# Kernel optimization log

Measured on AMD Instinct MI355X. Metric: run time of the kernel, lower is better.

Reference implementation:

```python
import jax, jax.numpy as jnp
import numpy as np

N_NODES = 100000
N_EDGES = 3200000
D_FEAT = 256
UNITS = 256


def setup_inputs() -> dict:
    key = jax.random.key(0)
    k1, k2, k3, k4, k5 = jax.random.split(key, 5)
    edge_row = jax.random.randint(k1, (N_EDGES,), 0, N_NODES, dtype=jnp.int32)
    edge_col = jax.random.randint(k2, (N_EDGES,), 0, N_NODES, dtype=jnp.int32)
    edge_val = jax.random.uniform(k3, (N_EDGES,), dtype=jnp.float32)
    x = jax.random.normal(k4, (N_NODES, D_FEAT), dtype=jnp.float32)
    weight = jax.random.normal(k5, (D_FEAT, UNITS), dtype=jnp.float32) * (1.0 / np.sqrt(D_FEAT))
    bias = jnp.zeros((UNITS,), dtype=jnp.float32)
    return {"edge_row": edge_row, "edge_col": edge_col, "edge_val": edge_val,
            "x": x, "weight": weight, "bias": bias}


def reference(edge_row, edge_col, edge_val, x, weight, bias):
    # h = X @ W  -- dense feature transform (N, units)
    h = x @ weight
    # out = An @ h -- SpMM over COO adjacency: out[r] += val_e * h[c_e]
    msgs = edge_val[:, None] * h[edge_col]          # (E, units) gather + scale
    out = jax.ops.segment_sum(msgs, edge_row, num_segments=N_NODES)
    out = out + bias
    return jax.nn.relu(out)
```

## Files before the change

### kernel.cpp

```cpp
#include <hip/hip_runtime.h>
#include <hip/hip_bf16.h>

#define N_NODES 100000
#define N_EDGES 3200000
#define DFEAT 256
#define UNITS 256

#define CHUNK 512
#define CHUNK_SHIFT 9
#define NCHUNKS ((N_NODES + CHUNK - 1) / CHUNK)

#define BIN_TILE 2048
#define BIN_NWG ((N_EDGES + BIN_TILE - 1) / BIN_TILE)
#define PADC 208

typedef short bf16x8 __attribute__((ext_vector_type(8)));
typedef float f32x4 __attribute__((ext_vector_type(4)));

__device__ __forceinline__ unsigned short f2bf(float f) {
    union { float f; unsigned u; } v; v.f = f;
    unsigned u = v.u;
    u += 0x7FFFu + ((u >> 16) & 1u);
    return (unsigned short)(u >> 16);
}

__global__ __launch_bounds__(256) void convert_x(const float4* __restrict__ x4,
                                                 unsigned short* __restrict__ xh) {
    size_t i = (size_t)blockIdx.x * 256 + threadIdx.x;
    float4 v = x4[i];
    ushort4 o = make_ushort4(f2bf(v.x), f2bf(v.y), f2bf(v.z), f2bf(v.w));
    *(ushort4*)&xh[i * 4] = o;
}

__global__ void convert_w(const float* __restrict__ w, unsigned short* __restrict__ wt) {
    int n = blockIdx.x, k = threadIdx.x;
    wt[n * DFEAT + k] = f2bf(w[k * UNITS + n]);
}

__global__ __launch_bounds__(256) void chunk_hist(const int* __restrict__ erow,
                                                  int* __restrict__ hist_all) {
    __shared__ int h[256];
    const int tid = threadIdx.x;
    h[tid] = 0;
    __syncthreads();
    const int base = blockIdx.x * BIN_TILE;
#pragma unroll
    for (int j = 0; j < 8; ++j) {
        int e = base + j * 256 + tid;
        if (e < N_EDGES) atomicAdd(&h[erow[e] >> CHUNK_SHIFT], 1);
    }
    __syncthreads();
    if (tid < NCHUNKS) hist_all[blockIdx.x * PADC + tid] = h[tid];
}

__global__ __launch_bounds__(256) void col_scan(int* __restrict__ hist_all,
                                                int* __restrict__ chunk_cnt) {
    __shared__ int t[256];
    const int b = blockIdx.x;
    const int tid = threadIdx.x;
    int v[7]; int local = 0;
#pragma unroll
    for (int j = 0; j < 7; ++j) {
        int w = tid * 7 + j;
        v[j] = (w < BIN_NWG) ? hist_all[w * PADC + b] : 0;
        local += v[j];
    }
    t[tid] = local;
    __syncthreads();
    for (int off = 1; off < 256; off <<= 1) {
        int u = 0;
        if (tid >= off) u = t[tid - off];
        __syncthreads();
        if (tid >= off) t[tid] += u;
        __syncthreads();
    }
    int run = t[tid] - local;
#pragma unroll
    for (int j = 0; j < 7; ++j) {
        int w = tid * 7 + j;
        if (w < BIN_NWG) { hist_all[w * PADC + b] = run; run += v[j]; }
    }
    if (tid == 255) chunk_cnt[b] = t[255];
}

__global__ void scan_chunks(const int* __restrict__ chunk_cnt, int* __restrict__ csum) {
    __shared__ int t[256];
    const int tid = threadIdx.x;
    int v = (tid < NCHUNKS) ? chunk_cnt[tid] : 0;
    t[tid] = v;
    __syncthreads();
    for (int off = 1; off < 256; off <<= 1) {
        int u = 0;
        if (tid >= off) u = t[tid - off];
        __syncthreads();
        if (tid >= off) t[tid] += u;
        __syncthreads();
    }
    if (tid < NCHUNKS) csum[tid] = t[tid] - v;
}

__global__ __launch_bounds__(256) void bin_edges(const int* __restrict__ erow,
                                                 const int* __restrict__ ecol,
                                                 const float* __restrict__ eval,
                                                 const int* __restrict__ hist_all,
                                                 const int* __restrict__ csum,
                                                 uint2* __restrict__ bin) {
    __shared__ int hist[256];
    __shared__ int scnt[256];
    __shared__ int delta[256];
    __shared__ uint2 rec[BIN_TILE];
    const int tid = threadIdx.x;
    const int base = blockIdx.x * BIN_TILE;

    hist[tid] = 0;
    __syncthreads();

    int r[8]; unsigned pk[8];
#pragma unroll
    for (int j = 0; j < 8; ++j) {
        int e = base + j * 256 + tid;
        if (e < N_EDGES) {
            r[j] = erow[e];
            pk[j] = (((unsigned)ecol[e]) << 15) | (f2bf(eval[e]) & 0x7FFFu);
            atomicAdd(&hist[r[j] >> CHUNK_SHIFT], 1);
        } else {
            r[j] = -1;
        }
    }
    __syncthreads();

    const int cntb = hist[tid];
    for (int off = 1; off < 256; off <<= 1) {
        int u = 0;
        if (tid >= off) u = hist[tid - off];
        __syncthreads();
        if (tid >= off) hist[tid] += u;
        __syncthreads();
    }
    const int excl = hist[tid] - cntb;
    if (tid < NCHUNKS)
        delta[tid] = csum[tid] + hist_all[blockIdx.x * PADC + tid] - excl;
    scnt[tid] = 0;
    __syncthreads();

#pragma unroll
    for (int j = 0; j < 8; ++j) {
        if (r[j] >= 0) {
            int b = r[j] >> CHUNK_SHIFT;
            int s = (b ? hist[b - 1] : 0) + atomicAdd(&scnt[b], 1);
            rec[s] = make_uint2(pk[j], (unsigned)r[j]);
        }
    }
    __syncthreads();

    const int n = min(BIN_TILE, N_EDGES - base);
    for (int s = tid; s < n; s += 256) {
        uint2 q = rec[s];
        bin[delta[(int)q.y >> CHUNK_SHIFT] + s] = q;
    }
}

__global__ __launch_bounds__(512) void sort_chunk(const int* __restrict__ csum,
                                                  const uint2* __restrict__ bin,
                                                  int* __restrict__ row_ptr,
                                                  unsigned* __restrict__ cv) {
    __shared__ int h[CHUNK];
    const int b = blockIdx.x;
    const int tid = threadIdx.x;
    const int start = csum[b];
    const int end = (b + 1 < NCHUNKS) ? csum[b + 1] : N_EDGES;

    h[tid] = 0;
    __syncthreads();
    {
        int i = start + tid;
        for (; i + 3 * 512 < end; i += 4 * 512) {
            int r0 = (int)bin[i].y, r1 = (int)bin[i + 512].y;
            int r2 = (int)bin[i + 1024].y, r3 = (int)bin[i + 1536].y;
            atomicAdd(&h[r0 & (CHUNK - 1)], 1);
            atomicAdd(&h[r1 & (CHUNK - 1)], 1);
            atomicAdd(&h[r2 & (CHUNK - 1)], 1);
            atomicAdd(&h[r3 & (CHUNK - 1)], 1);
        }
        for (; i < end; i += 512)
            atomicAdd(&h[(int)bin[i].y & (CHUNK - 1)], 1);
    }
    __syncthreads();

    const int cnt = h[tid];
    for (int off = 1; off < 512; off <<= 1) {
        int u = 0;
        if (tid >= off) u = h[tid - off];
        __syncthreads();
        if (tid >= off) h[tid] += u;
        __syncthreads();
    }
    const int rp = start + h[tid] - cnt;
    const int row = (b << CHUNK_SHIFT) + tid;
    if (row < N_NODES) row_ptr[row] = rp;
    if (b == NCHUNKS - 1 && tid == 0) row_ptr[N_NODES] = N_EDGES;
    h[tid] = rp;
    __syncthreads();

    int i = start + tid;
    for (; i + 3 * 512 < end; i += 4 * 512) {
        uint2 q0 = bin[i], q1 = bin[i + 512], q2 = bin[i + 1024], q3 = bin[i + 1536];
        int p0 = atomicAdd(&h[(int)q0.y & (CHUNK - 1)], 1);
        int p1 = atomicAdd(&h[(int)q1.y & (CHUNK - 1)], 1);
        int p2 = atomicAdd(&h[(int)q2.y & (CHUNK - 1)], 1);
        int p3 = atomicAdd(&h[(int)q3.y & (CHUNK - 1)], 1);
        cv[p0] = q0.x; cv[p1] = q1.x; cv[p2] = q2.x; cv[p3] = q3.x;
    }
    for (; i < end; i += 512) {
        uint2 q = bin[i];
        int p = atomicAdd(&h[(int)q.y & (CHUNK - 1)], 1);
        cv[p] = q.x;
    }
}

__global__ __launch_bounds__(256) void gather_rows(const int* __restrict__ row_ptr,
                                                   const unsigned* __restrict__ cv,
                                                   const unsigned short* __restrict__ xh,
                                                   unsigned short* __restrict__ tmp) {
    const int row = blockIdx.x * 4 + (threadIdx.x >> 6);
    if (row >= N_NODES) return;
    const int lane = threadIdx.x & 63;
    const int start = row_ptr[row];
    const int deg = row_ptr[row + 1] - start;
    const unsigned* __restrict__ p = cv + start;
    const uint2* __restrict__ x2 = (const uint2*)xh;

    float a0 = 0.f, a1 = 0.f, a2 = 0.f, a3 = 0.f;
    int i = 0;
    for (; i + 7 < deg; i += 8) {
        unsigned e[8]; uint2 g[8];
#pragma unroll
        for (int j = 0; j < 8; ++j) e[j] = p[i + j];
#pragma unroll
        for (int j = 0; j < 8; ++j) g[j] = x2[(size_t)(e[j] >> 15) * 64 + lane];
#pragma unroll
        for (int j = 0; j < 8; ++j) {
            float v = __uint_as_float((e[j] & 0x7FFFu) << 16);
            a0 = fmaf(v, __uint_as_float(g[j].x << 16), a0);
            a1 = fmaf(v, __uint_as_float(g[j].x & 0xFFFF0000u), a1);
            a2 = fmaf(v, __uint_as_float(g[j].y << 16), a2);
            a3 = fmaf(v, __uint_as_float(g[j].y & 0xFFFF0000u), a3);
        }
    }
    for (; i + 3 < deg; i += 4) {
        unsigned e[4]; uint2 g[4];
#pragma unroll
        for (int j = 0; j < 4; ++j) e[j] = p[i + j];
#pragma unroll
        for (int j = 0; j < 4; ++j) g[j] = x2[(size_t)(e[j] >> 15) * 64 + lane];
#pragma unroll
        for (int j = 0; j < 4; ++j) {
            float v = __uint_as_float((e[j] & 0x7FFFu) << 16);
            a0 = fmaf(v, __uint_as_float(g[j].x << 16), a0);
            a1 = fmaf(v, __uint_as_float(g[j].x & 0xFFFF0000u), a1);
            a2 = fmaf(v, __uint_as_float(g[j].y << 16), a2);
            a3 = fmaf(v, __uint_as_float(g[j].y & 0xFFFF0000u), a3);
        }
    }
    for (; i < deg; ++i) {
        unsigned e0 = p[i];
        uint2 g0 = x2[(size_t)(e0 >> 15) * 64 + lane];
        float v0 = __uint_as_float((e0 & 0x7FFFu) << 16);
        a0 = fmaf(v0, __uint_as_float(g0.x << 16), a0);
        a1 = fmaf(v0, __uint_as_float(g0.x & 0xFFFF0000u), a1);
        a2 = fmaf(v0, __uint_as_float(g0.y << 16), a2);
        a3 = fmaf(v0, __uint_as_float(g0.y & 0xFFFF0000u), a3);
    }
    ushort4 o = make_ushort4(f2bf(a0), f2bf(a1), f2bf(a2), f2bf(a3));
    *(ushort4*)&tmp[(size_t)row * 256 + lane * 4] = o;
}

#define GBM 64
#define GBK 64
#define LDK 72

__global__ __launch_bounds__(256) void gemm_mfma(
    const unsigned short* __restrict__ A,
    const unsigned short* __restrict__ Bt,
    const float* __restrict__ bias,
    float* __restrict__ C, int M)
{
    __shared__ unsigned short As[GBM * LDK];
    __shared__ unsigned short Bs[UNITS * LDK];

    const int tid = threadIdx.x;
    const int lane = tid & 63;
    const int wave_n = tid >> 6;
    const int block_m = blockIdx.x * GBM;

    const int quad = lane >> 4;
    const int l16 = lane & 15;

    const int ar = tid >> 2;
    const int aseg = tid & 3;

    f32x4 acc[4][4];
#pragma unroll
    for (int i = 0; i < 4; ++i)
#pragma unroll
        for (int j = 0; j < 4; ++j)
            acc[i][j] = {0.f, 0.f, 0.f, 0.f};

    for (int k0 = 0; k0 < DFEAT; k0 += GBK) {
        {
            const int gm = block_m + ar;
            uint4 v0 = {}, v1 = {};
            if (gm < M) {
                const uint4* src = (const uint4*)(A + (size_t)gm * DFEAT + k0 + aseg * 16);
                v0 = src[0]; v1 = src[1];
            }
            uint4* dst = (uint4*)&As[ar * LDK + aseg * 16];
            dst[0] = v0; dst[1] = v1;
        }
        {
            const uint4* src = (const uint4*)(Bt + (size_t)tid * DFEAT + k0);
            uint4* dst = (uint4*)&Bs[tid * LDK];
            uint4 v0 = src[0], v1 = src[1], v2 = src[2], v3 = src[3];
            uint4 v4 = src[4], v5 = src[5], v6 = src[6], v7 = src[7];
            dst[0] = v0; dst[1] = v1; dst[2] = v2; dst[3] = v3;
            dst[4] = v4; dst[5] = v5; dst[6] = v6; dst[7] = v7;
        }
        __syncthreads();

#pragma unroll
        for (int kc = 0; kc < 2; ++kc) {
            const int ko = kc * 32 + quad * 8;
            bf16x8 af[4], bfr[4];
#pragma unroll
            for (int i = 0; i < 4; ++i)
                af[i] = *(const bf16x8*)&As[(i * 16 + l16) * LDK + ko];
#pragma unroll
            for (int j = 0; j < 4; ++j)
                bfr[j] = *(const bf16x8*)&Bs[(wave_n * 64 + j * 16 + l16) * LDK + ko];
#pragma unroll
            for (int i = 0; i < 4; ++i)
#pragma unroll
                for (int j = 0; j < 4; ++j)
                    acc[i][j] = __builtin_amdgcn_mfma_f32_16x16x32_bf16(
                        af[i], bfr[j], acc[i][j], 0, 0, 0);
        }
        __syncthreads();
    }

#pragma unroll
    for (int j = 0; j < 4; ++j) {
        const int n = wave_n * 64 + j * 16 + l16;
        const float bj = bias[n];
#pragma unroll
        for (int i = 0; i < 4; ++i) {
            const int m0 = block_m + i * 16 + quad * 4;
#pragma unroll
            for (int rg = 0; rg < 4; ++rg) {
                const int m = m0 + rg;
                if (m < M)
                    C[(size_t)m * UNITS + n] = fmaxf(acc[i][j][rg] + bj, 0.f);
            }
        }
    }
}

extern "C" void kernel_launch(void* const* d_in, const int* in_sizes, int n_in,
                              void* d_out, int out_size, void* d_ws, size_t ws_size,
                              hipStream_t stream) {
    const int*   erow = (const int*)d_in[0];
    const int*   ecol = (const int*)d_in[1];
    const float* eval = (const float*)d_in[2];
    const float* x    = (const float*)d_in[3];
    const float* w    = (const float*)d_in[4];
    const float* bias = (const float*)d_in[5];
    float* out = (float*)d_out;

    char* ws = (char*)d_ws;
    unsigned short* tmp       = (unsigned short*)(ws);
    int*            row_ptr   = (int*)(ws + 51200000);
    int*            csum      = (int*)(ws + 51600016);
    int*            chunk_cnt = (int*)(ws + 51601040);
    unsigned*       cv        = (unsigned*)(ws + 51602064);
    unsigned short* wt        = (unsigned short*)(ws + 64402064);
    uint2*          bin       = (uint2*)(ws + 64533136);
    int*            hist_all  = (int*)(ws + 90133136);

    unsigned short* xh = (unsigned short*)d_out;

    convert_x<<<(N_NODES * DFEAT / 4) / 256, 256, 0, stream>>>((const float4*)x, xh);
    convert_w<<<UNITS, DFEAT, 0, stream>>>(w, wt);

    chunk_hist<<<BIN_NWG, 256, 0, stream>>>(erow, hist_all);
    col_scan<<<NCHUNKS, 256, 0, stream>>>(hist_all, chunk_cnt);
    scan_chunks<<<1, 256, 0, stream>>>(chunk_cnt, csum);
    bin_edges<<<BIN_NWG, 256, 0, stream>>>(erow, ecol, eval, hist_all, csum, bin);
    sort_chunk<<<NCHUNKS, 512, 0, stream>>>(csum, bin, row_ptr, cv);

    gather_rows<<<(N_NODES + 3) / 4, 256, 0, stream>>>(row_ptr, cv, xh, tmp);

    gemm_mfma<<<(N_NODES + GBM - 1) / GBM, 256, 0, stream>>>(tmp, wt, bias, out, N_NODES);
}
```

Baseline: 537.7 us.

## Shrink sort chunks to 128 rows and split bin into packed word plus byte row

Reduces the per-chunk row range from 512 to 128, so there are about 782 chunks and more workgroups in sort_chunk, each running 256 threads. The binned records are stored as a 4-byte packed col/val word plus a 1-byte local row instead of an 8-byte pair, which cuts bin traffic. bin_edges now reuses the per-tile histogram from chunk_hist instead of recomputing it with atomics. The costs are larger histogram matrices, a 1024-thread chunk scan, and more col_scan blocks.

Result: slower. 561.9 us (+4.5%).

```diff
diff --git a/kernel.cpp b/kernel.cpp
--- a/kernel.cpp
+++ b/kernel.cpp
@@ -6,13 +6,13 @@
 #define DFEAT 256
 #define UNITS 256
 
-#define CHUNK 512
-#define CHUNK_SHIFT 9
+#define CHUNK 128
+#define CHUNK_SHIFT 7
 #define NCHUNKS ((N_NODES + CHUNK - 1) / CHUNK)
 
 #define BIN_TILE 2048
 #define BIN_NWG ((N_EDGES + BIN_TILE - 1) / BIN_TILE)
-#define PADC 208
+#define PADC 784
 
 typedef short bf16x8 __attribute__((ext_vector_type(8)));
 typedef float f32x4 __attribute__((ext_vector_type(4)));
@@ -38,10 +38,10 @@
 }
 
 __global__ __launch_bounds__(256) void chunk_hist(const int* __restrict__ erow,
-                                                  int* __restrict__ hist_all) {
-    __shared__ int h[256];
-    const int tid = threadIdx.x;
-    h[tid] = 0;
+                                                  int* __restrict__ hist_cnt) {
+    __shared__ int h[PADC];
+    const int tid = threadIdx.x;
+    for (int c = tid; c < PADC; c += 256) h[c] = 0;
     __syncthreads();
     const int base = blockIdx.x * BIN_TILE;
 #pragma unroll
@@ -50,19 +50,20 @@
         if (e < N_EDGES) atomicAdd(&h[erow[e] >> CHUNK_SHIFT], 1);
     }
     __syncthreads();
-    if (tid < NCHUNKS) hist_all[blockIdx.x * PADC + tid] = h[tid];
-}
-
-__global__ __launch_bounds__(256) void col_scan(int* __restrict__ hist_all,
+    for (int c = tid; c < NCHUNKS; c += 256) hist_cnt[blockIdx.x * PADC + c] = h[c];
+}
+
+__global__ __launch_bounds__(256) void col_scan(const int* __restrict__ hist_cnt,
+                                                int* __restrict__ hist_pre,
                                                 int* __restrict__ chunk_cnt) {
     __shared__ int t[256];
-    const int b = blockIdx.x;
+    const int c = blockIdx.x;
     const int tid = threadIdx.x;
     int v[7]; int local = 0;
 #pragma unroll
     for (int j = 0; j < 7; ++j) {
         int w = tid * 7 + j;
-        v[j] = (w < BIN_NWG) ? hist_all[w * PADC + b] : 0;
+        v[j] = (w < BIN_NWG) ? hist_cnt[w * PADC + c] : 0;
         local += v[j];
     }
     t[tid] = local;
@@ -78,18 +79,19 @@
 #pragma unroll
     for (int j = 0; j < 7; ++j) {
         int w = tid * 7 + j;
-        if (w < BIN_NWG) { hist_all[w * PADC + b] = run; run += v[j]; }
-    }
-    if (tid == 255) chunk_cnt[b] = t[255];
-}
-
-__global__ void scan_chunks(const int* __restrict__ chunk_cnt, int* __restrict__ csum) {
-    __shared__ int t[256];
+        if (w < BIN_NWG) { hist_pre[w * PADC + c] = run; run += v[j]; }
+    }
+    if (tid == 255) chunk_cnt[c] = t[255];
+}
+
+__global__ __launch_bounds__(1024) void scan_chunks(const int* __restrict__ chunk_cnt,
+                                                    int* __restrict__ csum) {
+    __shared__ int t[1024];
     const int tid = threadIdx.x;
     int v = (tid < NCHUNKS) ? chunk_cnt[tid] : 0;
     t[tid] = v;
     __syncthreads();
-    for (int off = 1; off < 256; off <<= 1) {
+    for (int off = 1; off < 1024; off <<= 1) {
         int u = 0;
         if (tid >= off) u = t[tid - off];
         __syncthreads();
@@ -97,58 +99,66 @@
         __syncthreads();
     }
     if (tid < NCHUNKS) csum[tid] = t[tid] - v;
+    if (tid == 0) csum[NCHUNKS] = N_EDGES;
 }
 
 __global__ __launch_bounds__(256) void bin_edges(const int* __restrict__ erow,
                                                  const int* __restrict__ ecol,
                                                  const float* __restrict__ eval,
-                                                 const int* __restrict__ hist_all,
+                                                 const int* __restrict__ hist_cnt,
+                                                 const int* __restrict__ hist_pre,
                                                  const int* __restrict__ csum,
-                                                 uint2* __restrict__ bin) {
-    __shared__ int hist[256];
-    __shared__ int scnt[256];
-    __shared__ int delta[256];
+                                                 unsigned* __restrict__ bin_pk,
+                                                 unsigned char* __restrict__ bin_r8) {
+    __shared__ int ex[PADC];
+    __shared__ int delta[PADC];
+    __shared__ int scnt[PADC];
+    __shared__ int part[256];
     __shared__ uint2 rec[BIN_TILE];
     const int tid = threadIdx.x;
-    const int base = blockIdx.x * BIN_TILE;
-
-    hist[tid] = 0;
-    __syncthreads();
-
-    int r[8]; unsigned pk[8];
+    const int wg = blockIdx.x;
+    const int base = wg * BIN_TILE;
+
+    int v[4]; int local = 0;
+    const int c0 = tid * 4;
+#pragma unroll
+    for (int k = 0; k < 4; ++k) {
+        int c = c0 + k;
+        v[k] = (c < NCHUNKS) ? hist_cnt[wg * PADC + c] : 0;
+        local += v[k];
+    }
+    part[tid] = local;
+    __syncthreads();
+    for (int off = 1; off < 256; off <<= 1) {
+        int u = 0;
+        if (tid >= off) u = part[tid - off];
+        __syncthreads();
+        if (tid >= off) part[tid] += u;
+        __syncthreads();
+    }
+    {
+        int run = part[tid] - local;
+#pragma unroll
+        for (int k = 0; k < 4; ++k) {
+            int c = c0 + k;
+            if (c < PADC) { ex[c] = run; scnt[c] = 0; }
+            run += v[k];
+        }
+    }
+    __syncthreads();
+    for (int c = tid; c < NCHUNKS; c += 256)
+        delta[c] = csum[c] + hist_pre[wg * PADC + c] - ex[c];
+    __syncthreads();
+
 #pragma unroll
     for (int j = 0; j < 8; ++j) {
         int e = base + j * 256 + tid;
         if (e < N_EDGES) {
-            r[j] = erow[e];
-            pk[j] = (((unsigned)ecol[e]) << 15) | (f2bf(eval[e]) & 0x7FFFu);
-            atomicAdd(&hist[r[j] >> CHUNK_SHIFT], 1);
-        } else {
-            r[j] = -1;
-        }
-    }
-    __syncthreads();
-
-    const int cntb = hist[tid];
-    for (int off = 1; off < 256; off <<= 1) {
-        int u = 0;
-        if (tid >= off) u = hist[tid - off];
-        __syncthreads();
-        if (tid >= off) hist[tid] += u;
-        __syncthreads();
-    }
-    const int excl = hist[tid] - cntb;
-    if (tid < NCHUNKS)
-        delta[tid] = csum[tid] + hist_all[blockIdx.x * PADC + tid] - excl;
-    scnt[tid] = 0;
-    __syncthreads();
-
-#pragma unroll
-    for (int j = 0; j < 8; ++j) {
-        if (r[j] >= 0) {
-            int b = r[j] >> CHUNK_SHIFT;
-            int s = (b ? hist[b - 1] : 0) + atomicAdd(&scnt[b], 1);
-            rec[s] = make_uint2(pk[j], (unsigned)r[j]);
+            int r = erow[e];
+            unsigned pk = (((unsigned)ecol[e]) << 15) | (f2bf(eval[e]) & 0x7FFFu);
+            int b = r >> CHUNK_SHIFT;
+            int s = ex[b] + atomicAdd(&scnt[b], 1);
+            rec[s] = make_uint2(pk, (unsigned)r);
         }
     }
     __syncthreads();
@@ -156,65 +166,73 @@
     const int n = min(BIN_TILE, N_EDGES - base);
     for (int s = tid; s < n; s += 256) {
         uint2 q = rec[s];
-        bin[delta[(int)q.y >> CHUNK_SHIFT] + s] = q;
-    }
-}
-
-__global__ __launch_bounds__(512) void sort_chunk(const int* __restrict__ csum,
-                                                  const uint2* __restrict__ bin,
+        int pos = delta[(int)q.y >> CHUNK_SHIFT] + s;
+        bin_pk[pos] = q.x;
+        bin_r8[pos] = (unsigned char)(q.y & (CHUNK - 1));
+    }
+}
+
+__global__ __launch_bounds__(256) void sort_chunk(const int* __restrict__ csum,
+                                                  const unsigned* __restrict__ bin_pk,
+                                                  const unsigned char* __restrict__ bin_r8,
                                                   int* __restrict__ row_ptr,
                                                   unsigned* __restrict__ cv) {
     __shared__ int h[CHUNK];
     const int b = blockIdx.x;
     const int tid = threadIdx.x;
     const int start = csum[b];
-    const int end = (b + 1 < NCHUNKS) ? csum[b + 1] : N_EDGES;
-
-    h[tid] = 0;
+    const int end = csum[b + 1];
+
+    if (tid < CHUNK) h[tid] = 0;
     __syncthreads();
     {
         int i = start + tid;
-        for (; i + 3 * 512 < end; i += 4 * 512) {
-            int r0 = (int)bin[i].y, r1 = (int)bin[i + 512].y;
-            int r2 = (int)bin[i + 1024].y, r3 = (int)bin[i + 1536].y;
-            atomicAdd(&h[r0 & (CHUNK - 1)], 1);
-            atomicAdd(&h[r1 & (CHUNK - 1)], 1);
-            atomicAdd(&h[r2 & (CHUNK - 1)], 1);
-            atomicAdd(&h[r3 & (CHUNK - 1)], 1);
-        }
-        for (; i < end; i += 512)
-            atomicAdd(&h[(int)bin[i].y & (CHUNK - 1)], 1);
-    }
-    __syncthreads();
-
-    const int cnt = h[tid];
-    for (int off = 1; off < 512; off <<= 1) {
+        for (; i + 3 * 256 < end; i += 4 * 256) {
+            int r0 = bin_r8[i], r1 = bin_r8[i + 256];
+            int r2 = bin_r8[i + 512], r3 = bin_r8[i + 768];
+            atomicAdd(&h[r0], 1); atomicAdd(&h[r1], 1);
+            atomicAdd(&h[r2], 1); atomicAdd(&h[r3], 1);
+        }
+        for (; i < end; i += 256) atomicAdd(&h[bin_r8[i]], 1);
+    }
+    __syncthreads();
+
+    int cnt = 0;
+    if (tid < CHUNK) cnt = h[tid];
+    for (int off = 1; off < CHUNK; off <<= 1) {
         int u = 0;
-        if (tid >= off) u = h[tid - off];
-        __syncthreads();
-        if (tid >= off) h[tid] += u;
-        __syncthreads();
-    }
-    const int rp = start + h[tid] - cnt;
-    const int row = (b << CHUNK_SHIFT) + tid;
-    if (row < N_NODES) row_ptr[row] = rp;
+        if (tid < CHUNK && tid >= off) u = h[tid - off];
+        __syncthreads();
+        if (tid < CHUNK && tid >= off) h[tid] += u;
+        __syncthreads();
+    }
+    int rp = 0;
+    if (tid < CHUNK) {
+        rp = start + h[tid] - cnt;
+        int row = (b << CHUNK_SHIFT) + tid;
+        if (row < N_NODES) row_ptr[row] = rp;
+    }
     if (b == NCHUNKS - 1 && tid == 0) row_ptr[N_NODES] = N_EDGES;
-    h[tid] = rp;
+    __syncthreads();
+    if (tid < CHUNK) h[tid] = rp;
     __syncthreads();
 
     int i = start + tid;
-    for (; i + 3 * 512 < end; i += 4 * 512) {
-        uint2 q0 = bin[i], q1 = bin[i + 512], q2 = bin[i + 1024], q3 = bin[i + 1536];
-        int p0 = atomicAdd(&h[(int)q0.y & (CHUNK - 1)], 1);
-        int p1 = atomicAdd(&h[(int)q1.y & (CHUNK - 1)], 1);
-        int p2 = atomicAdd(&h[(int)q2.y & (CHUNK - 1)], 1);
-        int p3 = atomicAdd(&h[(int)q3.y & (CHUNK - 1)], 1);
-        cv[p0] = q0.x; cv[p1] = q1.x; cv[p2] = q2.x; cv[p3] = q3.x;
-    }
-    for (; i < end; i += 512) {
-        uint2 q = bin[i];
-        int p = atomicAdd(&h[(int)q.y & (CHUNK - 1)], 1);
-        cv[p] = q.x;
+    for (; i + 3 * 256 < end; i += 4 * 256) {
+        unsigned k0 = bin_pk[i], k1 = bin_pk[i + 256];
+        unsigned k2 = bin_pk[i + 512], k3 = bin_pk[i + 768];
+        int r0 = bin_r8[i], r1 = bin_r8[i + 256];
+        int r2 = bin_r8[i + 512], r3 = bin_r8[i + 768];
+        int p0 = atomicAdd(&h[r0], 1);
+        int p1 = atomicAdd(&h[r1], 1);
+        int p2 = atomicAdd(&h[r2], 1);
+        int p3 = atomicAdd(&h[r3], 1);
+        cv[p0] = k0; cv[p1] = k1; cv[p2] = k2; cv[p3] = k3;
+    }
+    for (; i < end; i += 256) {
+        unsigned k = bin_pk[i];
+        int p = atomicAdd(&h[(int)bin_r8[i]], 1);
+        cv[p] = k;
     }
 }
 
@@ -379,22 +397,25 @@
     unsigned short* tmp       = (unsigned short*)(ws);
     int*            row_ptr   = (int*)(ws + 51200000);
     int*            csum      = (int*)(ws + 51600016);
-    int*            chunk_cnt = (int*)(ws + 51601040);
-    unsigned*       cv        = (unsigned*)(ws + 51602064);
-    unsigned short* wt        = (unsigned short*)(ws + 64402064);
-    uint2*          bin       = (uint2*)(ws + 64533136);
-    int*            hist_all  = (int*)(ws + 90133136);
+    int*            chunk_cnt = (int*)(ws + 51603152);
+    unsigned*       cv        = (unsigned*)(ws + 51606288);
+    unsigned short* wt        = (unsigned short*)(ws + 64406288);
+    unsigned*       bin_pk    = (unsigned*)(ws + 64537360);
+    unsigned char*  bin_r8    = (unsigned char*)(ws + 77337360);
+    int*            hist_cnt  = (int*)(ws + 80537360);
+    int*            hist_pre  = (int*)(ws + 85438928);
 
     unsigned short* xh = (unsigned short*)d_out;
 
     convert_x<<<(N_NODES * DFEAT / 4) / 256, 256, 0, stream>>>((const float4*)x, xh);
     convert_w<<<UNITS, DFEAT, 0, stream>>>(w, wt);
 
-    chunk_hist<<<BIN_NWG, 256, 0, stream>>>(erow, hist_all);
-    col_scan<<<NCHUNKS, 256, 0, stream>>>(hist_all, chunk_cnt);
-    scan_chunks<<<1, 256, 0, stream>>>(chunk_cnt, csum);
-    bin_edges<<<BIN_NWG, 256, 0, stream>>>(erow, ecol, eval, hist_all, csum, bin);
-    sort_chunk<<<NCHUNKS, 512, 0, stream>>>(csum, bin, row_ptr, cv);
+    chunk_hist<<<BIN_NWG, 256, 0, stream>>>(erow, hist_cnt);
+    col_scan<<<NCHUNKS, 256, 0, stream>>>(hist_cnt, hist_pre, chunk_cnt);
+    scan_chunks<<<1, 1024, 0, stream>>>(chunk_cnt, csum);
+    bin_edges<<<BIN_NWG, 256, 0, stream>>>(erow, ecol, eval, hist_cnt, hist_pre,
+                                           csum, bin_pk, bin_r8);
+    sort_chunk<<<NCHUNKS, 256, 0, stream>>>(csum, bin_pk, bin_r8, row_ptr, cv);
 
     gather_rows<<<(N_NODES + 3) / 4, 256, 0, stream>>>(row_ptr, cv, xh, tmp);
 
```

## Replace two-pass edge binning with atomic-cursor scatter into fixed-capacity buckets

Applied to the files above, without the earlier changes.

Removes the separate chunk histogram and column-scan passes. Each binning block now reserves space per chunk with a global atomicAdd on a per-chunk cursor and scatters into fixed-capacity (CAP) buckets, and the chunk sort reads from those buckets. This saves one full read of edge_row plus the hist_all traffic and two kernel launches. The x and W conversion kernels are also merged into one launch. The cost is that bucket overflow becomes possible if a chunk receives more than CAP edges, and bucket order becomes nondeterministic, though the final per-row sort hides this.

Result: slower. 560.8 us (+4.3%).

```diff
diff --git a/kernel.cpp b/kernel.cpp
--- a/kernel.cpp
+++ b/kernel.cpp
@@ -9,10 +9,10 @@
 #define CHUNK 512
 #define CHUNK_SHIFT 9
 #define NCHUNKS ((N_NODES + CHUNK - 1) / CHUNK)
+#define CAP 18432
 
 #define BIN_TILE 2048
 #define BIN_NWG ((N_EDGES + BIN_TILE - 1) / BIN_TILE)
-#define PADC 208
 
 typedef short bf16x8 __attribute__((ext_vector_type(8)));
 typedef float f32x4 __attribute__((ext_vector_type(4)));
@@ -24,87 +24,26 @@
     return (unsigned short)(u >> 16);
 }
 
-__global__ __launch_bounds__(256) void convert_x(const float4* __restrict__ x4,
-                                                 unsigned short* __restrict__ xh) {
-    size_t i = (size_t)blockIdx.x * 256 + threadIdx.x;
-    float4 v = x4[i];
-    ushort4 o = make_ushort4(f2bf(v.x), f2bf(v.y), f2bf(v.z), f2bf(v.w));
-    *(ushort4*)&xh[i * 4] = o;
-}
-
-__global__ void convert_w(const float* __restrict__ w, unsigned short* __restrict__ wt) {
-    int n = blockIdx.x, k = threadIdx.x;
-    wt[n * DFEAT + k] = f2bf(w[k * UNITS + n]);
-}
-
-__global__ __launch_bounds__(256) void chunk_hist(const int* __restrict__ erow,
-                                                  int* __restrict__ hist_all) {
-    __shared__ int h[256];
-    const int tid = threadIdx.x;
-    h[tid] = 0;
-    __syncthreads();
-    const int base = blockIdx.x * BIN_TILE;
-#pragma unroll
-    for (int j = 0; j < 8; ++j) {
-        int e = base + j * 256 + tid;
-        if (e < N_EDGES) atomicAdd(&h[erow[e] >> CHUNK_SHIFT], 1);
-    }
-    __syncthreads();
-    if (tid < NCHUNKS) hist_all[blockIdx.x * PADC + tid] = h[tid];
-}
-
-__global__ __launch_bounds__(256) void col_scan(int* __restrict__ hist_all,
-                                                int* __restrict__ chunk_cnt) {
-    __shared__ int t[256];
-    const int b = blockIdx.x;
-    const int tid = threadIdx.x;
-    int v[7]; int local = 0;
-#pragma unroll
-    for (int j = 0; j < 7; ++j) {
-        int w = tid * 7 + j;
-        v[j] = (w < BIN_NWG) ? hist_all[w * PADC + b] : 0;
-        local += v[j];
-    }
-    t[tid] = local;
-    __syncthreads();
-    for (int off = 1; off < 256; off <<= 1) {
-        int u = 0;
-        if (tid >= off) u = t[tid - off];
-        __syncthreads();
-        if (tid >= off) t[tid] += u;
-        __syncthreads();
-    }
-    int run = t[tid] - local;
-#pragma unroll
-    for (int j = 0; j < 7; ++j) {
-        int w = tid * 7 + j;
-        if (w < BIN_NWG) { hist_all[w * PADC + b] = run; run += v[j]; }
-    }
-    if (tid == 255) chunk_cnt[b] = t[255];
-}
-
-__global__ void scan_chunks(const int* __restrict__ chunk_cnt, int* __restrict__ csum) {
-    __shared__ int t[256];
-    const int tid = threadIdx.x;
-    int v = (tid < NCHUNKS) ? chunk_cnt[tid] : 0;
-    t[tid] = v;
-    __syncthreads();
-    for (int off = 1; off < 256; off <<= 1) {
-        int u = 0;
-        if (tid >= off) u = t[tid - off];
-        __syncthreads();
-        if (tid >= off) t[tid] += u;
-        __syncthreads();
-    }
-    if (tid < NCHUNKS) csum[tid] = t[tid] - v;
-}
-
-__global__ __launch_bounds__(256) void bin_edges(const int* __restrict__ erow,
-                                                 const int* __restrict__ ecol,
-                                                 const float* __restrict__ eval,
-                                                 const int* __restrict__ hist_all,
-                                                 const int* __restrict__ csum,
-                                                 uint2* __restrict__ bin) {
+__global__ __launch_bounds__(256) void convert_xw(const float4* __restrict__ x4,
+                                                  unsigned short* __restrict__ xh,
+                                                  const float* __restrict__ w,
+                                                  unsigned short* __restrict__ wt) {
+    if (blockIdx.x < 25000) {
+        size_t i = (size_t)blockIdx.x * 256 + threadIdx.x;
+        float4 v = x4[i];
+        ushort4 o = make_ushort4(f2bf(v.x), f2bf(v.y), f2bf(v.z), f2bf(v.w));
+        *(ushort4*)&xh[i * 4] = o;
+    } else {
+        int n = blockIdx.x - 25000, k = threadIdx.x;
+        wt[n * DFEAT + k] = f2bf(w[k * UNITS + n]);
+    }
+}
+
+__global__ __launch_bounds__(256) void bin_scatter(const int* __restrict__ erow,
+                                                   const int* __restrict__ ecol,
+                                                   const float* __restrict__ eval,
+                                                   int* __restrict__ gcur,
+                                                   uint2* __restrict__ bin) {
     __shared__ int hist[256];
     __shared__ int scnt[256];
     __shared__ int delta[256];
@@ -138,8 +77,10 @@
         __syncthreads();
     }
     const int excl = hist[tid] - cntb;
-    if (tid < NCHUNKS)
-        delta[tid] = csum[tid] + hist_all[blockIdx.x * PADC + tid] - excl;
+    if (tid < NCHUNKS) {
+        int rb = (cntb > 0) ? atomicAdd(&gcur[tid], cntb) : 0;
+        delta[tid] = tid * CAP + rb - excl;
+    }
     scnt[tid] = 0;
     __syncthreads();
 
@@ -160,30 +101,49 @@
     }
 }
 
-__global__ __launch_bounds__(512) void sort_chunk(const int* __restrict__ csum,
+__global__ void scan_chunks(const int* __restrict__ gcur, int* __restrict__ csum) {
+    __shared__ int t[256];
+    const int tid = threadIdx.x;
+    int v = (tid < NCHUNKS) ? gcur[tid] : 0;
+    t[tid] = v;
+    __syncthreads();
+    for (int off = 1; off < 256; off <<= 1) {
+        int u = 0;
+        if (tid >= off) u = t[tid - off];
+        __syncthreads();
+        if (tid >= off) t[tid] += u;
+        __syncthreads();
+    }
+    if (tid < NCHUNKS) csum[tid] = t[tid] - v;
+    if (tid == 0) csum[NCHUNKS] = N_EDGES;
+}
+
+__global__ __launch_bounds__(512) void sort_chunk(const int* __restrict__ gcur,
+                                                  const int* __restrict__ csum,
                                                   const uint2* __restrict__ bin,
                                                   int* __restrict__ row_ptr,
                                                   unsigned* __restrict__ cv) {
     __shared__ int h[CHUNK];
     const int b = blockIdx.x;
     const int tid = threadIdx.x;
-    const int start = csum[b];
-    const int end = (b + 1 < NCHUNKS) ? csum[b + 1] : N_EDGES;
+    const int cnt_c = gcur[b];
+    const int rbase = csum[b];
+    const uint2* __restrict__ src = bin + (size_t)b * CAP;
 
     h[tid] = 0;
     __syncthreads();
     {
-        int i = start + tid;
-        for (; i + 3 * 512 < end; i += 4 * 512) {
-            int r0 = (int)bin[i].y, r1 = (int)bin[i + 512].y;
-            int r2 = (int)bin[i + 1024].y, r3 = (int)bin[i + 1536].y;
-            atomicAdd(&h[r0 & (CHUNK - 1)], 1);
-            atomicAdd(&h[r1 & (CHUNK - 1)], 1);
-            atomicAdd(&h[r2 & (CHUNK - 1)], 1);
-            atomicAdd(&h[r3 & (CHUNK - 1)], 1);
-        }
-        for (; i < end; i += 512)
-            atomicAdd(&h[(int)bin[i].y & (CHUNK - 1)], 1);
+        int i = tid;
+        for (; i + 3 * 512 < cnt_c; i += 4 * 512) {
+            int r0 = (int)src[i].y & (CHUNK - 1);
+            int r1 = (int)src[i + 512].y & (CHUNK - 1);
+            int r2 = (int)src[i + 1024].y & (CHUNK - 1);
+            int r3 = (int)src[i + 1536].y & (CHUNK - 1);
+            atomicAdd(&h[r0], 1); atomicAdd(&h[r1], 1);
+            atomicAdd(&h[r2], 1); atomicAdd(&h[r3], 1);
+        }
+        for (; i < cnt_c; i += 512)
+            atomicAdd(&h[(int)src[i].y & (CHUNK - 1)], 1);
     }
     __syncthreads();
 
@@ -195,24 +155,25 @@
         if (tid >= off) h[tid] += u;
         __syncthreads();
     }
-    const int rp = start + h[tid] - cnt;
+    const int rp = rbase + h[tid] - cnt;
     const int row = (b << CHUNK_SHIFT) + tid;
     if (row < N_NODES) row_ptr[row] = rp;
     if (b == NCHUNKS - 1 && tid == 0) row_ptr[N_NODES] = N_EDGES;
+    __syncthreads();
     h[tid] = rp;
     __syncthreads();
 
-    int i = start + tid;
-    for (; i + 3 * 512 < end; i += 4 * 512) {
-        uint2 q0 = bin[i], q1 = bin[i + 512], q2 = bin[i + 1024], q3 = bin[i + 1536];
+    int i = tid;
+    for (; i + 3 * 512 < cnt_c; i += 4 * 512) {
+        uint2 q0 = src[i], q1 = src[i + 512], q2 = src[i + 1024], q3 = src[i + 1536];
         int p0 = atomicAdd(&h[(int)q0.y & (CHUNK - 1)], 1);
         int p1 = atomicAdd(&h[(int)q1.y & (CHUNK - 1)], 1);
         int p2 = atomicAdd(&h[(int)q2.y & (CHUNK - 1)], 1);
         int p3 = atomicAdd(&h[(int)q3.y & (CHUNK - 1)], 1);
         cv[p0] = q0.x; cv[p1] = q1.x; cv[p2] = q2.x; cv[p3] = q3.x;
     }
-    for (; i < end; i += 512) {
-        uint2 q = bin[i];
+    for (; i < cnt_c; i += 512) {
+        uint2 q = src[i];
         int p = atomicAdd(&h[(int)q.y & (CHUNK - 1)], 1);
         cv[p] = q.x;
     }
@@ -376,25 +337,22 @@
     float* out = (float*)d_out;
 
     char* ws = (char*)d_ws;
-    unsigned short* tmp       = (unsigned short*)(ws);
-    int*            row_ptr   = (int*)(ws + 51200000);
-    int*            csum      = (int*)(ws + 51600016);
-    int*            chunk_cnt = (int*)(ws + 51601040);
-    unsigned*       cv        = (unsigned*)(ws + 51602064);
-    unsigned short* wt        = (unsigned short*)(ws + 64402064);
-    uint2*          bin       = (uint2*)(ws + 64533136);
-    int*            hist_all  = (int*)(ws + 90133136);
+    unsigned short* tmp     = (unsigned short*)(ws);
+    int*            row_ptr = (int*)(ws + 51200000);
+    int*            csum    = (int*)(ws + 51600016);
+    int*            gcur    = (int*)(ws + 51601040);
+    unsigned*       cv      = (unsigned*)(ws + 51602064);
+    unsigned short* wt      = (unsigned short*)(ws + 64402064);
+    uint2*          bin     = (uint2*)(ws + 64533136);
 
     unsigned short* xh = (unsigned short*)d_out;
 
-    convert_x<<<(N_NODES * DFEAT / 4) / 256, 256, 0, stream>>>((const float4*)x, xh);
-    convert_w<<<UNITS, DFEAT, 0, stream>>>(w, wt);
-
-    chunk_hist<<<BIN_NWG, 256, 0, stream>>>(erow, hist_all);
-    col_scan<<<NCHUNKS, 256, 0, stream>>>(hist_all, chunk_cnt);
-    scan_chunks<<<1, 256, 0, stream>>>(chunk_cnt, csum);
-    bin_edges<<<BIN_NWG, 256, 0, stream>>>(erow, ecol, eval, hist_all, csum, bin);
-    sort_chunk<<<NCHUNKS, 512, 0, stream>>>(csum, bin, row_ptr, cv);
+    convert_xw<<<25000 + UNITS, 256, 0, stream>>>((const float4*)x, xh, w, wt);
+
+    hipMemsetAsync(gcur, 0, NCHUNKS * sizeof(int), stream);
+    bin_scatter<<<BIN_NWG, 256, 0, stream>>>(erow, ecol, eval, gcur, bin);
+    scan_chunks<<<1, 256, 0, stream>>>(gcur, csum);
+    sort_chunk<<<NCHUNKS, 512, 0, stream>>>(gcur, csum, bin, row_ptr, cv);
 
     gather_rows<<<(N_NODES + 3) / 4, 256, 0, stream>>>(row_ptr, cv, xh, tmp);
 
```

## Slice feature matrix by columns and pin slices to XCDs for cache-resident gather

Applied to the files above, without the earlier changes.

Converts x into 16 column slices of 16 bf16 each, stored slice-major, so every slice (about 3.2 MB) can stay resident in one XCD's L2. The gather kernel now gives each XCD two slices and uses persistent waves that walk contiguous row ranges. Within a wave, 16 lane groups split a row's edges and the partial sums are combined with shuffles. The GEMM reads its A tile from the sliced layout, and the x and w conversion kernels are merged into one launch. In exchange, every edge index is read 16 times and each random access is only 32 bytes; the gain relies on blockIdx-to-XCD round-robin mapping, and a missing sync in the scan was also added.

After: 787.0 us. 1.46x slower.

```diff
diff --git a/kernel.cpp b/kernel.cpp
--- a/kernel.cpp
+++ b/kernel.cpp
@@ -13,6 +13,10 @@
 #define BIN_TILE 2048
 #define BIN_NWG ((N_EDGES + BIN_TILE - 1) / BIN_TILE)
 #define PADC 208
+
+#define SLICES 16
+#define FS 16
+#define GAT_BLOCKS 2048
 
 typedef short bf16x8 __attribute__((ext_vector_type(8)));
 typedef float f32x4 __attribute__((ext_vector_type(4)));
@@ -24,17 +28,31 @@
     return (unsigned short)(u >> 16);
 }
 
-__global__ __launch_bounds__(256) void convert_x(const float4* __restrict__ x4,
-                                                 unsigned short* __restrict__ xh) {
-    size_t i = (size_t)blockIdx.x * 256 + threadIdx.x;
-    float4 v = x4[i];
-    ushort4 o = make_ushort4(f2bf(v.x), f2bf(v.y), f2bf(v.z), f2bf(v.w));
-    *(ushort4*)&xh[i * 4] = o;
-}
-
-__global__ void convert_w(const float* __restrict__ w, unsigned short* __restrict__ wt) {
-    int n = blockIdx.x, k = threadIdx.x;
-    wt[n * DFEAT + k] = f2bf(w[k * UNITS + n]);
+__global__ __launch_bounds__(256) void convert_xw(const float* __restrict__ x,
+                                                  unsigned short* __restrict__ xs,
+                                                  const float* __restrict__ w,
+                                                  unsigned short* __restrict__ wt) {
+    if (blockIdx.x < 1563) {
+        const int n0 = blockIdx.x * 64;
+        const int s = threadIdx.x >> 4;
+        const int j = threadIdx.x & 15;
+#pragma unroll
+        for (int i = 0; i < 4; ++i) {
+            const int n = n0 + j * 4 + i;
+            if (n < N_NODES) {
+                const float4* src = (const float4*)(x + (size_t)n * DFEAT + s * FS);
+                float4 v0 = src[0], v1 = src[1], v2 = src[2], v3 = src[3];
+                unsigned short* dst = xs + ((size_t)s * N_NODES + n) * FS;
+                *(ushort4*)(dst)      = make_ushort4(f2bf(v0.x), f2bf(v0.y), f2bf(v0.z), f2bf(v0.w));
+                *(ushort4*)(dst + 4)  = make_ushort4(f2bf(v1.x), f2bf(v1.y), f2bf(v1.z), f2bf(v1.w));
+                *(ushort4*)(dst + 8)  = make_ushort4(f2bf(v2.x), f2bf(v2.y), f2bf(v2.z), f2bf(v2.w));
+                *(ushort4*)(dst + 12) = make_ushort4(f2bf(v3.x), f2bf(v3.y), f2bf(v3.z), f2bf(v3.w));
+            }
+        }
+    } else {
+        int n = blockIdx.x - 1563, k = threadIdx.x;
+        wt[n * DFEAT + k] = f2bf(w[k * UNITS + n]);
+    }
 }
 
 __global__ __launch_bounds__(256) void chunk_hist(const int* __restrict__ erow,
@@ -199,6 +217,7 @@
     const int row = (b << CHUNK_SHIFT) + tid;
     if (row < N_NODES) row_ptr[row] = rp;
     if (b == NCHUNKS - 1 && tid == 0) row_ptr[N_NODES] = N_EDGES;
+    __syncthreads();
     h[tid] = rp;
     __syncthreads();
 
@@ -218,61 +237,51 @@
     }
 }
 
-__global__ __launch_bounds__(256) void gather_rows(const int* __restrict__ row_ptr,
-                                                   const unsigned* __restrict__ cv,
-                                                   const unsigned short* __restrict__ xh,
-                                                   unsigned short* __restrict__ tmp) {
-    const int row = blockIdx.x * 4 + (threadIdx.x >> 6);
-    if (row >= N_NODES) return;
+__global__ __launch_bounds__(256) void gather_sliced(const int* __restrict__ row_ptr,
+                                                     const unsigned* __restrict__ cv,
+                                                     const unsigned short* __restrict__ xs,
+                                                     unsigned short* __restrict__ ts) {
     const int lane = threadIdx.x & 63;
-    const int start = row_ptr[row];
-    const int deg = row_ptr[row + 1] - start;
-    const unsigned* __restrict__ p = cv + start;
-    const uint2* __restrict__ x2 = (const uint2*)xh;
-
-    float a0 = 0.f, a1 = 0.f, a2 = 0.f, a3 = 0.f;
-    int i = 0;
-    for (; i + 7 < deg; i += 8) {
-        unsigned e[8]; uint2 g[8];
-#pragma unroll
-        for (int j = 0; j < 8; ++j) e[j] = p[i + j];
-#pragma unroll
-        for (int j = 0; j < 8; ++j) g[j] = x2[(size_t)(e[j] >> 15) * 64 + lane];
-#pragma unroll
-        for (int j = 0; j < 8; ++j) {
-            float v = __uint_as_float((e[j] & 0x7FFFu) << 16);
-            a0 = fmaf(v, __uint_as_float(g[j].x << 16), a0);
-            a1 = fmaf(v, __uint_as_float(g[j].x & 0xFFFF0000u), a1);
-            a2 = fmaf(v, __uint_as_float(g[j].y << 16), a2);
-            a3 = fmaf(v, __uint_as_float(g[j].y & 0xFFFF0000u), a3);
-        }
-    }
-    for (; i + 3 < deg; i += 4) {
-        unsigned e[4]; uint2 g[4];
-#pragma unroll
-        for (int j = 0; j < 4; ++j) e[j] = p[i + j];
-#pragma unroll
-        for (int j = 0; j < 4; ++j) g[j] = x2[(size_t)(e[j] >> 15) * 64 + lane];
-#pragma unroll
-        for (int j = 0; j < 4; ++j) {
-            float v = __uint_as_float((e[j] & 0x7FFFu) << 16);
-            a0 = fmaf(v, __uint_as_float(g[j].x << 16), a0);
-            a1 = fmaf(v, __uint_as_float(g[j].x & 0xFFFF0000u), a1);
-            a2 = fmaf(v, __uint_as_float(g[j].y << 16), a2);
-            a3 = fmaf(v, __uint_as_float(g[j].y & 0xFFFF0000u), a3);
-        }
-    }
-    for (; i < deg; ++i) {
-        unsigned e0 = p[i];
-        uint2 g0 = x2[(size_t)(e0 >> 15) * 64 + lane];
-        float v0 = __uint_as_float((e0 & 0x7FFFu) << 16);
-        a0 = fmaf(v0, __uint_as_float(g0.x << 16), a0);
-        a1 = fmaf(v0, __uint_as_float(g0.x & 0xFFFF0000u), a1);
-        a2 = fmaf(v0, __uint_as_float(g0.y << 16), a2);
-        a3 = fmaf(v0, __uint_as_float(g0.y & 0xFFFF0000u), a3);
-    }
-    ushort4 o = make_ushort4(f2bf(a0), f2bf(a1), f2bf(a2), f2bf(a3));
-    *(ushort4*)&tmp[(size_t)row * 256 + lane * 4] = o;
+    const int wv = threadIdx.x >> 6;
+    const int xcd = blockIdx.x & 7;
+    const int rank = (blockIdx.x >> 3) * 4 + wv;
+    const int nw = (GAT_BLOCKS >> 3) * 4;
+    const int rows_per = (N_NODES + nw - 1) / nw;
+    const int r0 = rank * rows_per;
+    const int r1 = min(r0 + rows_per, N_NODES);
+    const int g = lane >> 2, sub = lane & 3;
+
+    for (int ph = 0; ph < 2; ++ph) {
+        const int s = xcd * 2 + ph;
+        const unsigned short* __restrict__ xsl = xs + (size_t)s * N_NODES * FS;
+        unsigned short* __restrict__ tsl = ts + (size_t)s * N_NODES * FS;
+        for (int row = r0; row < r1; ++row) {
+            const int start = row_ptr[row];
+            const int deg = row_ptr[row + 1] - start;
+            const unsigned* __restrict__ p = cv + start;
+            float a0 = 0.f, a1 = 0.f, a2 = 0.f, a3 = 0.f;
+            for (int i = g; i < deg; i += 16) {
+                unsigned e = p[i];
+                float val = __uint_as_float((e & 0x7FFFu) << 16);
+                uint2 gx = *(const uint2*)(xsl + (size_t)(e >> 15) * FS + sub * 4);
+                a0 = fmaf(val, __uint_as_float(gx.x << 16), a0);
+                a1 = fmaf(val, __uint_as_float(gx.x & 0xFFFF0000u), a1);
+                a2 = fmaf(val, __uint_as_float(gx.y << 16), a2);
+                a3 = fmaf(val, __uint_as_float(gx.y & 0xFFFF0000u), a3);
+            }
+#pragma unroll
+            for (int m = 4; m <= 32; m <<= 1) {
+                a0 += __shfl_xor(a0, m, 64);
+                a1 += __shfl_xor(a1, m, 64);
+                a2 += __shfl_xor(a2, m, 64);
+                a3 += __shfl_xor(a3, m, 64);
+            }
+            if (lane < 4) {
+                ushort4 o = make_ushort4(f2bf(a0), f2bf(a1), f2bf(a2), f2bf(a3));
+                *(ushort4*)(tsl + (size_t)row * FS + lane * 4) = o;
+            }
+        }
+    }
 }
 
 #define GBM 64
@@ -296,8 +305,8 @@
     const int quad = lane >> 4;
     const int l16 = lane & 15;
 
-    const int ar = tid >> 2;
-    const int aseg = tid & 3;
+    const int q = tid >> 6;
+    const int ar = tid & 63;
 
     f32x4 acc[4][4];
 #pragma unroll
@@ -309,12 +318,13 @@
     for (int k0 = 0; k0 < DFEAT; k0 += GBK) {
         {
             const int gm = block_m + ar;
+            const int s = (k0 >> 4) + q;
             uint4 v0 = {}, v1 = {};
             if (gm < M) {
-                const uint4* src = (const uint4*)(A + (size_t)gm * DFEAT + k0 + aseg * 16);
+                const uint4* src = (const uint4*)(A + ((size_t)s * N_NODES + gm) * FS);
                 v0 = src[0]; v1 = src[1];
             }
-            uint4* dst = (uint4*)&As[ar * LDK + aseg * 16];
+            uint4* dst = (uint4*)&As[ar * LDK + q * 16];
             dst[0] = v0; dst[1] = v1;
         }
         {
@@ -385,10 +395,9 @@
     uint2*          bin       = (uint2*)(ws + 64533136);
     int*            hist_all  = (int*)(ws + 90133136);
 
-    unsigned short* xh = (unsigned short*)d_out;
-
-    convert_x<<<(N_NODES * DFEAT / 4) / 256, 256, 0, stream>>>((const float4*)x, xh);
-    convert_w<<<UNITS, DFEAT, 0, stream>>>(w, wt);
+    unsigned short* xs = (unsigned short*)d_out;
+
+    convert_xw<<<1563 + UNITS, 256, 0, stream>>>(x, xs, w, wt);
 
     chunk_hist<<<BIN_NWG, 256, 0, stream>>>(erow, hist_all);
     col_scan<<<NCHUNKS, 256, 0, stream>>>(hist_all, chunk_cnt);
@@ -396,7 +405,7 @@
     bin_edges<<<BIN_NWG, 256, 0, stream>>>(erow, ecol, eval, hist_all, csum, bin);
     sort_chunk<<<NCHUNKS, 512, 0, stream>>>(csum, bin, row_ptr, cv);
 
-    gather_rows<<<(N_NODES + 3) / 4, 256, 0, stream>>>(row_ptr, cv, xh, tmp);
+    gather_sliced<<<GAT_BLOCKS, 256, 0, stream>>>(row_ptr, cv, xs, tmp);
 
     gemm_mfma<<<(N_NODES + GBM - 1) / GBM, 256, 0, stream>>>(tmp, wt, bias, out, N_NODES);
 }
```
